# Optimization experiments

Hardware: AMD Instinct MI355X
Metric: run time of the kernel (lower is better)

The kernel has to match this reference:

```python
import jax, jax.numpy as jnp
import numpy as np

HEAD_NUM = 16
KEY_DIM = 64
EMBED = 1024
KV_OUT = HEAD_NUM * KEY_DIM  # 1024


def setup_inputs() -> dict:
    key = jax.random.key(0)
    ks = jax.random.split(key, 11)
    B, L, E = 2, 2048, EMBED
    scale = 0.02
    return {
        "query": jax.random.normal(ks[0], (B, L, E), jnp.float32),
        "key": jax.random.normal(ks[1], (B, L, E), jnp.float32),
        "value": jax.random.normal(ks[2], (B, L, E), jnp.float32),
        "W_Query": jax.random.normal(ks[3], (E, KV_OUT), jnp.float32) * scale,
        "W_Key": jax.random.normal(ks[4], (E, KV_OUT), jnp.float32) * scale,
        "W_Value": jax.random.normal(ks[5], (E, KV_OUT), jnp.float32) * scale,
        "W_Output": jax.random.normal(ks[6], (KV_OUT, E), jnp.float32) * scale,
        "B_Query": jnp.zeros((KV_OUT,), jnp.float32),
        "B_Key": jnp.zeros((KV_OUT,), jnp.float32),
        "B_Value": jnp.zeros((KV_OUT,), jnp.float32),
        "B_Output": jnp.zeros((E,), jnp.float32),
    }


def reference(query, key, value, W_Query, W_Key, W_Value, W_Output,
              B_Query, B_Key, B_Value, B_Output):
    B, Lq, E = query.shape
    Lk = key.shape[1]
    H, D = HEAD_NUM, KEY_DIM
    # QKV projections + bias
    q = query @ W_Query + B_Query            # [B, Lq, H*D]
    k = key @ W_Key + B_Key                  # [B, Lk, H*D]
    v = value @ W_Value + B_Value            # [B, Lk, H*D]
    # tf.split(axis=2) per head == reshape to [B, L, H, D]
    q = q.reshape(B, Lq, H, D)
    k = k.reshape(B, Lk, H, D)
    v = v.reshape(B, Lk, H, D)
    # scaled dot-product attention (no mask, dropout=0)
    scores = jnp.einsum("bqhd,bkhd->bhqk", q, k) / (D ** 0.5)
    probs = jax.nn.softmax(scores, axis=-1)
    out = jnp.einsum("bhqk,bkhd->bqhd", probs, v)  # [B, Lq, H, D]
    out = out.reshape(B, Lq, H * D)
    return out @ W_Output + B_Output
```

## Files before the change

kernel.cpp:

```cpp
#include <hip/hip_runtime.h>

using u16 = unsigned short;
using u32 = unsigned int;

typedef __attribute__((ext_vector_type(8))) short bf16x8;
typedef __attribute__((ext_vector_type(4))) float f32x4;
typedef __attribute__((ext_vector_type(4))) u32 u32x4;
typedef __attribute__((ext_vector_type(2))) u32 u32x2;
typedef __attribute__((ext_vector_type(4))) _Float16 f16x4;

#define MFMA_BF16_K32(a, b, c) __builtin_amdgcn_mfma_f32_16x16x32_bf16((a), (b), (c), 0, 0, 0)
#define MFMA_F16_K16(a, b, c) __builtin_amdgcn_mfma_f32_16x16x16f16((a), (b), (c), 0, 0, 0)

#define QSCALE 0.18033688011112042f

extern "C" __device__ float __ocml_native_exp2_f32(float);

__device__ __forceinline__ u16 f2bf(float f) {
  u32 u = __builtin_bit_cast(u32, f);
  return (u16)((u + 0x7fffu + ((u >> 16) & 1u)) >> 16);
}

__device__ __forceinline__ u32 pk_f16(float a, float b) {
  auto v = __builtin_amdgcn_cvt_pkrtz(a, b);
  return __builtin_bit_cast(u32, v);
}

__device__ __forceinline__ void load_lds16(const void* g, void* l) {
  __builtin_amdgcn_global_load_lds((__attribute__((address_space(1))) void*)g,
                                   (__attribute__((address_space(3))) void*)l,
                                   16, 0, 0);
}

__global__ __launch_bounds__(256) void cvt_all_kernel(
    const float* __restrict__ q, const float* __restrict__ k, const float* __restrict__ v,
    u16* __restrict__ oq, u16* __restrict__ ok, u16* __restrict__ ov,
    const float* __restrict__ w0, const float* __restrict__ w1,
    const float* __restrict__ w2, const float* __restrict__ w3,
    u16* __restrict__ d0, u16* __restrict__ d1,
    u16* __restrict__ d2, u16* __restrict__ d3) {
  const int id = blockIdx.x;
  const int tid = threadIdx.x;
  if (id < 6144) {
    const int z = id >> 11, bx = id & 2047;
    const float* s = z == 0 ? q : z == 1 ? k : v;
    u16* d = z == 0 ? oq : z == 1 ? ok : ov;
    int i = (bx * 256 + tid) * 8;
    f32x4 a = *(const f32x4*)(s + i);
    f32x4 b = *(const f32x4*)(s + i + 4);
    u32x4 o;
    o.x = (u32)f2bf(a.x) | ((u32)f2bf(a.y) << 16);
    o.y = (u32)f2bf(a.z) | ((u32)f2bf(a.w) << 16);
    o.z = (u32)f2bf(b.x) | ((u32)f2bf(b.y) << 16);
    o.w = (u32)f2bf(b.z) | ((u32)f2bf(b.w) << 16);
    *(u32x4*)(d + i) = o;
    return;
  }
  __shared__ float t[64][65];
  const int r0 = id - 6144;
  const int z = r0 >> 8, rr0 = r0 & 255;
  const int bx = rr0 & 15, by = rr0 >> 4;
  const float* src = z == 0 ? w0 : z == 1 ? w1 : z == 2 ? w2 : w3;
  u16* dst = z == 0 ? d0 : z == 1 ? d1 : z == 2 ? d2 : d3;
  const float scale = (z == 0) ? QSCALE : 1.0f;
  const int r = tid >> 4, c4 = (tid & 15) * 4;
#pragma unroll
  for (int i = 0; i < 4; ++i) {
    int row = r + i * 16;
    f32x4 vv = *(const f32x4*)(src + (by * 64 + row) * 1024 + bx * 64 + c4);
    t[row][c4 + 0] = vv.x;
    t[row][c4 + 1] = vv.y;
    t[row][c4 + 2] = vv.z;
    t[row][c4 + 3] = vv.w;
  }
  __syncthreads();
  const int rw = tid >> 2, cc = (tid & 3) * 16;
  alignas(16) u16 tmp[16];
#pragma unroll
  for (int j = 0; j < 16; ++j) tmp[j] = f2bf(t[cc + j][rw] * scale);
  u32x4* outp = (u32x4*)(dst + (bx * 64 + rw) * 1024 + by * 64 + cc);
  outp[0] = *(const u32x4*)&tmp[0];
  outp[1] = *(const u32x4*)&tmp[8];
}

__global__ __launch_bounds__(256) void gemm_qkv_kernel(
    const u16* __restrict__ x0, const u16* __restrict__ x1, const u16* __restrict__ x2,
    const u16* __restrict__ w0, const u16* __restrict__ w1, const u16* __restrict__ w2,
    const float* __restrict__ b0, const float* __restrict__ b1, const float* __restrict__ b2,
    u16* __restrict__ c0, u16* __restrict__ c1, u16* __restrict__ vt) {
  __shared__ u16 As[128 * 64];
  __shared__ u16 Bs[128 * 64];
  const int lid = blockIdx.x;
  const int xcd = lid & 7, rr = lid >> 3;
  const int nb = rr & 7, slot = rr >> 3;
  const int g = slot * 8 + xcd;
  const int z = g >> 5, m_idx = g & 31;
  const u16* A = z == 0 ? x0 : z == 1 ? x1 : x2;
  const u16* Bt = z == 0 ? w0 : z == 1 ? w1 : w2;
  const float* bias = z == 0 ? b0 : z == 1 ? b1 : b2;
  const float bscale = z == 0 ? QSCALE : 1.0f;
  const int tid = threadIdx.x;
  const int wave = tid >> 6, lane = tid & 63;
  const int l16 = lane & 15, quad = lane >> 4;
  const int l7 = l16 & 7;
  const int wm = wave >> 1, wn = wave & 1;
  const int m0 = m_idx * 128, n0 = nb * 128;

  f32x4 acc[4][4];
  const f32x4 zf = {0.f, 0.f, 0.f, 0.f};
#pragma unroll
  for (int i = 0; i < 4; ++i)
#pragma unroll
    for (int j = 0; j < 4; ++j) acc[i][j] = zf;

  for (int kb = 0; kb < 1024; kb += 64) {
#pragma unroll
    for (int t = 0; t < 4; ++t) {
      int c = wave * 256 + t * 64 + lane;
      int row = c >> 3, sc8 = (c & 7) ^ (row & 7);
      load_lds16(A + (m0 + row) * 1024 + kb + sc8 * 8, &As[(wave * 256 + t * 64) * 8]);
    }
#pragma unroll
    for (int t = 0; t < 4; ++t) {
      int c = wave * 256 + t * 64 + lane;
      int row = c >> 3, sc8 = (c & 7) ^ (row & 7);
      load_lds16(Bt + (n0 + row) * 1024 + kb + sc8 * 8, &Bs[(wave * 256 + t * 64) * 8]);
    }
    asm volatile("s_waitcnt vmcnt(0)" ::: "memory");
    __syncthreads();
#pragma unroll
    for (int ks = 0; ks < 2; ++ks) {
      const int sch = (ks * 4 + quad) ^ l7;
      bf16x8 af[4], bfv[4];
#pragma unroll
      for (int mt = 0; mt < 4; ++mt)
        af[mt] = *(const bf16x8*)&As[(wm * 64 + mt * 16 + l16) * 64 + sch * 8];
#pragma unroll
      for (int nt = 0; nt < 4; ++nt)
        bfv[nt] = *(const bf16x8*)&Bs[(wn * 64 + nt * 16 + l16) * 64 + sch * 8];
#pragma unroll
      for (int mt = 0; mt < 4; ++mt)
#pragma unroll
        for (int nt = 0; nt < 4; ++nt) acc[mt][nt] = MFMA_BF16_K32(af[mt], bfv[nt], acc[mt][nt]);
    }
    __syncthreads();
  }

  float bv[4];
#pragma unroll
  for (int nt = 0; nt < 4; ++nt) bv[nt] = bias[n0 + wn * 64 + nt * 16 + l16] * bscale;
  if (z != 2) {
    u16* C = z == 0 ? c0 : c1;
#pragma unroll
    for (int mt = 0; mt < 4; ++mt)
#pragma unroll
      for (int nt = 0; nt < 4; ++nt)
#pragma unroll
        for (int r = 0; r < 4; ++r) {
          int row = m0 + wm * 64 + mt * 16 + quad * 4 + r;
          int col = n0 + wn * 64 + nt * 16 + l16;
          C[row * 1024 + col] = f2bf(acc[mt][nt][r] + bv[nt]);
        }
  } else {
#pragma unroll
    for (int mt = 0; mt < 4; ++mt)
#pragma unroll
      for (int nt = 0; nt < 4; ++nt) {
        int kvb = m0 + wm * 64 + mt * 16 + quad * 4;
        int bb = kvb >> 11, kv = kvb & 2047;
        int col = n0 + wn * 64 + nt * 16 + l16;
        int h = col >> 6, dt = (col >> 4) & 3, ld = col & 15;
        int pair = bb * 16 + h;
        int kb2 = kv >> 7, chunk = (kv >> 4) & 7, qd = (kv >> 2) & 3;
        f16x4 hv;
#pragma unroll
        for (int r = 0; r < 4; ++r) hv[r] = (_Float16)(acc[mt][nt][r] + bv[nt]);
        u16* dst = vt + ((((pair * 16 + kb2) * 8 + chunk) * 4 + dt) * 256) + qd * 64 + ld * 4;
        *(f16x4*)dst = hv;
      }
  }
}

__global__ __launch_bounds__(256) void gemm_out_kernel(const u16* __restrict__ A,
                                                       const u16* __restrict__ Bt,
                                                       const float* __restrict__ bias,
                                                       float* __restrict__ C) {
  __shared__ u16 As[64 * 64];
  __shared__ u16 Bs[128 * 64];
  const int lid = blockIdx.x;
  const int xcd = lid & 7, rr = lid >> 3;
  const int nb = rr & 7, slot = rr >> 3;
  const int by = slot * 8 + xcd;
  const int tid = threadIdx.x;
  const int wave = tid >> 6, lane = tid & 63;
  const int l16 = lane & 15, quad = lane >> 4;
  const int l7 = l16 & 7;
  const int m0 = by * 64, n0 = nb * 128;

  f32x4 acc[4][2];
  const f32x4 zf = {0.f, 0.f, 0.f, 0.f};
#pragma unroll
  for (int i = 0; i < 4; ++i)
#pragma unroll
    for (int j = 0; j < 2; ++j) acc[i][j] = zf;

  for (int kb = 0; kb < 1024; kb += 64) {
#pragma unroll
    for (int t = 0; t < 2; ++t) {
      int c = wave * 128 + t * 64 + lane;
      int row = c >> 3, sc8 = (c & 7) ^ (row & 7);
      load_lds16(A + (m0 + row) * 1024 + kb + sc8 * 8, &As[(wave * 128 + t * 64) * 8]);
    }
#pragma unroll
    for (int t = 0; t < 4; ++t) {
      int c = wave * 256 + t * 64 + lane;
      int row = c >> 3, sc8 = (c & 7) ^ (row & 7);
      load_lds16(Bt + (n0 + row) * 1024 + kb + sc8 * 8, &Bs[(wave * 256 + t * 64) * 8]);
    }
    asm volatile("s_waitcnt vmcnt(0)" ::: "memory");
    __syncthreads();
#pragma unroll
    for (int ks = 0; ks < 2; ++ks) {
      const int sch = (ks * 4 + quad) ^ l7;
      bf16x8 af[4], bfv[2];
#pragma unroll
      for (int mt = 0; mt < 4; ++mt)
        af[mt] = *(const bf16x8*)&As[(mt * 16 + l16) * 64 + sch * 8];
#pragma unroll
      for (int nt = 0; nt < 2; ++nt)
        bfv[nt] = *(const bf16x8*)&Bs[(wave * 32 + nt * 16 + l16) * 64 + sch * 8];
#pragma unroll
      for (int mt = 0; mt < 4; ++mt)
#pragma unroll
        for (int nt = 0; nt < 2; ++nt) acc[mt][nt] = MFMA_BF16_K32(af[mt], bfv[nt], acc[mt][nt]);
    }
    __syncthreads();
  }

  float bv[2];
#pragma unroll
  for (int nt = 0; nt < 2; ++nt) bv[nt] = bias[n0 + wave * 32 + nt * 16 + l16];
#pragma unroll
  for (int mt = 0; mt < 4; ++mt)
#pragma unroll
    for (int nt = 0; nt < 2; ++nt)
#pragma unroll
      for (int r = 0; r < 4; ++r) {
        int row = m0 + mt * 16 + quad * 4 + r;
        int col = n0 + wave * 32 + nt * 16 + l16;
        C[row * 1024 + col] = acc[mt][nt][r] + bv[nt];
      }
}

union PU { u32 u[2]; f16x4 v; };

#define QK_EXP(CUR, PKV)                                                          \
  _Pragma("unroll") for (int c2 = 0; c2 < 2; ++c2) {                              \
    const int chunk = wave * 2 + c2;                                              \
    f32x4 s_acc[4];                                                               \
    _Pragma("unroll") for (int qn = 0; qn < 4; ++qn) s_acc[qn] = zf;              \
    _Pragma("unroll") for (int ks = 0; ks < 2; ++ks) {                            \
      bf16x8 kf = *(const bf16x8*)&k_lds[CUR][(chunk * 16 + l16) * 64 +           \
                                              ((ks * 4 + quad) ^ l7) * 8];        \
      _Pragma("unroll") for (int qn = 0; qn < 4; ++qn)                            \
        s_acc[qn] = MFMA_BF16_K32(kf, qf[qn][ks], s_acc[qn]);                     \
    }                                                                             \
    _Pragma("unroll") for (int qn = 0; qn < 4; ++qn) {                            \
      float e0 = __ocml_native_exp2_f32(s_acc[qn].x);                             \
      float e1 = __ocml_native_exp2_f32(s_acc[qn].y);                             \
      float e2 = __ocml_native_exp2_f32(s_acc[qn].z);                             \
      float e3 = __ocml_native_exp2_f32(s_acc[qn].w);                             \
      lp[qn] += (e0 + e1) + (e2 + e3);                                            \
      PKV[c2][qn].u[0] = pk_f16(e0, e1);                                          \
      PKV[c2][qn].u[1] = pk_f16(e2, e3);                                          \
    }                                                                             \
  }

#define FLASH_BODY(KB, CUR, VCUR, VNXT, PFV, PFK, WAIT)                           \
  {                                                                               \
    __builtin_amdgcn_s_barrier();                                                 \
    asm volatile("" ::: "memory");                                                \
    if (PFV) {                                                                    \
      const u16* vp = Vh + ((KB) + 1) * 8192;                                     \
      _Pragma("unroll") for (int c2 = 0; c2 < 2; ++c2)                            \
        _Pragma("unroll") for (int dt = 0; dt < 4; ++dt)                          \
          VNXT[c2][dt] =                                                          \
              *(const f16x4*)(vp + ((wave * 2 + c2) * 4 + dt) * 256 + lane * 4);  \
    }                                                                             \
    PU pkv[2][4];                                                                 \
    QK_EXP(CUR, pkv)                                                              \
    asm volatile("s_waitcnt lgkmcnt(0)" ::: "memory");                            \
    __builtin_amdgcn_s_barrier();                                                 \
    asm volatile("" ::: "memory");                                                \
    if (PFK) {                                                                    \
      const int kv0 = ((KB) + 2) * 128;                                           \
      _Pragma("unroll") for (int t = 0; t < 4; ++t) {                             \
        int c = (t * 4 + wave) * 64 + lane;                                       \
        int row = c >> 3, sc8 = (c & 7) ^ (row & 7);                              \
        load_lds16(Kh + (kv0 + row) * 1024 + sc8 * 8,                             \
                   &k_lds[CUR][((t * 4 + wave) * 64) * 8]);                       \
      }                                                                           \
    }                                                                             \
    WAIT;                                                                         \
    _Pragma("unroll") for (int c2 = 0; c2 < 2; ++c2)                              \
      _Pragma("unroll") for (int dt = 0; dt < 4; ++dt)                            \
        _Pragma("unroll") for (int qn = 0; qn < 4; ++qn)                          \
          o_acc[qn][dt] = MFMA_F16_K16(pkv[c2][qn].v, VCUR[c2][dt], o_acc[qn][dt]); \
  }

#define W12 asm volatile("s_waitcnt vmcnt(12)" ::: "memory")
#define W8 asm volatile("s_waitcnt vmcnt(8)" ::: "memory")
#define W0 asm volatile("s_waitcnt vmcnt(0)" ::: "memory")

__global__ __launch_bounds__(256, 2) void flash_kernel(const u16* __restrict__ Q,
                                                       const u16* __restrict__ K,
                                                       const u16* __restrict__ Vt,
                                                       u16* __restrict__ O) {
  __shared__ u16 k_lds[2][128 * 64];
  __shared__ float lred[4][64];
  __shared__ float lfin[64];
  const int tid = threadIdx.x;
  const int wave = tid >> 6, lane = tid & 63;
  const int l16 = lane & 15, quad = lane >> 4;
  const int l7 = l16 & 7;
  const int id = blockIdx.x;
  const int xcd = id & 7, slot = id >> 3;
  const int pair = xcd * 4 + (slot & 3);
  const int qb = slot >> 2;
  const int b = pair >> 4, h = pair & 15;
  const u16* Qh = Q + (b * 2048 + qb * 64) * 1024 + h * 64;
  const u16* Kh = K + b * 2048 * 1024 + h * 64;
  const u16* Vh = Vt + pair * 131072;

#pragma unroll
  for (int t = 0; t < 2; ++t) {
    int c = (t * 4 + wave) * 64 + lane;
    int row = c >> 3, sc8 = (c & 7) ^ (row & 7);
    load_lds16(Qh + row * 1024 + sc8 * 8, &k_lds[0][((t * 4 + wave) * 64) * 8]);
  }
  asm volatile("s_waitcnt vmcnt(0)" ::: "memory");
  __syncthreads();
  bf16x8 qf[4][2];
#pragma unroll
  for (int qn = 0; qn < 4; ++qn)
#pragma unroll
    for (int ks = 0; ks < 2; ++ks)
      qf[qn][ks] = *(const bf16x8*)&k_lds[0][(qn * 16 + l16) * 64 + (((ks * 4 + quad) ^ l7)) * 8];
  __syncthreads();

#pragma unroll
  for (int t = 0; t < 4; ++t) {
    int c = (t * 4 + wave) * 64 + lane;
    int row = c >> 3, sc8 = (c & 7) ^ (row & 7);
    load_lds16(Kh + row * 1024 + sc8 * 8, &k_lds[0][((t * 4 + wave) * 64) * 8]);
  }
  f16x4 vregA[2][4], vregB[2][4];
#pragma unroll
  for (int c2 = 0; c2 < 2; ++c2)
#pragma unroll
    for (int dt = 0; dt < 4; ++dt)
      vregA[c2][dt] = *(const f16x4*)(Vh + ((wave * 2 + c2) * 4 + dt) * 256 + lane * 4);
#pragma unroll
  for (int t = 0; t < 4; ++t) {
    int c = (t * 4 + wave) * 64 + lane;
    int row = c >> 3, sc8 = (c & 7) ^ (row & 7);
    load_lds16(Kh + (128 + row) * 1024 + sc8 * 8, &k_lds[1][((t * 4 + wave) * 64) * 8]);
  }
  W12;

  f32x4 o_acc[4][4];
  const f32x4 zf = {0.f, 0.f, 0.f, 0.f};
#pragma unroll
  for (int qn = 0; qn < 4; ++qn)
#pragma unroll
    for (int dt = 0; dt < 4; ++dt) o_acc[qn][dt] = zf;
  float lp[4] = {0.f, 0.f, 0.f, 0.f};

  for (int kb2 = 0; kb2 < 7; ++kb2) {
    const int kb = kb2 * 2;
    FLASH_BODY(kb, 0, vregA, vregB, true, true, W12);
    FLASH_BODY(kb + 1, 1, vregB, vregA, true, true, W12);
  }
  FLASH_BODY(14, 0, vregA, vregB, true, false, W8);
  FLASH_BODY(15, 1, vregB, vregA, false, false, W0);

#pragma unroll
  for (int qn = 0; qn < 4; ++qn) {
    lp[qn] += __shfl_xor(lp[qn], 16);
    lp[qn] += __shfl_xor(lp[qn], 32);
  }
  if (quad == 0) {
#pragma unroll
    for (int qn = 0; qn < 4; ++qn) lred[wave][qn * 16 + l16] = lp[qn];
  }
  float* bufA = (float*)&k_lds[0][0];
  float* bufB = (float*)&k_lds[1][0];
  if (wave == 1 || wave == 3) {
    float* buf = (wave == 1) ? bufA : bufB;
#pragma unroll
    for (int qm = 0; qm < 4; ++qm)
#pragma unroll
      for (int dt = 0; dt < 4; ++dt)
        *(f32x4*)&buf[(((qm * 4 + dt) * 4 + quad) * 16 + l16) * 4] = o_acc[qm][dt];
  }
  __syncthreads();
  if (tid < 64) lfin[tid] = lred[0][tid] + lred[1][tid] + lred[2][tid] + lred[3][tid];
  if (wave == 0 || wave == 2) {
    float* buf = (wave == 0) ? bufA : bufB;
#pragma unroll
    for (int qm = 0; qm < 4; ++qm)
#pragma unroll
      for (int dt = 0; dt < 4; ++dt)
        o_acc[qm][dt] += *(const f32x4*)&buf[(((qm * 4 + dt) * 4 + quad) * 16 + l16) * 4];
  }
  __syncthreads();
  if (wave == 2) {
#pragma unroll
    for (int qm = 0; qm < 4; ++qm)
#pragma unroll
      for (int dt = 0; dt < 4; ++dt)
        *(f32x4*)&bufA[(((qm * 4 + dt) * 4 + quad) * 16 + l16) * 4] = o_acc[qm][dt];
  }
  __syncthreads();
  if (wave == 0) {
#pragma unroll
    for (int qm = 0; qm < 4; ++qm)
#pragma unroll
      for (int dt = 0; dt < 4; ++dt)
        o_acc[qm][dt] += *(const f32x4*)&bufA[(((qm * 4 + dt) * 4 + quad) * 16 + l16) * 4];
#pragma unroll
    for (int qm = 0; qm < 4; ++qm)
#pragma unroll
      for (int r = 0; r < 4; ++r) {
        int qrow = qm * 16 + quad * 4 + r;
        float inv = 1.0f / lfin[qrow];
        int row = b * 2048 + qb * 64 + qrow;
#pragma unroll
        for (int dt = 0; dt < 4; ++dt)
          O[row * 1024 + h * 64 + dt * 16 + l16] = f2bf(o_acc[qm][dt][r] * inv);
      }
  }
}

extern "C" void kernel_launch(void* const* d_in, const int* in_sizes, int n_in,
                              void* d_out, int out_size, void* d_ws, size_t ws_size,
                              hipStream_t stream) {
  const float* q = (const float*)d_in[0];
  const float* k = (const float*)d_in[1];
  const float* v = (const float*)d_in[2];
  const float* Wq = (const float*)d_in[3];
  const float* Wk = (const float*)d_in[4];
  const float* Wv = (const float*)d_in[5];
  const float* Wo = (const float*)d_in[6];
  const float* Bq = (const float*)d_in[7];
  const float* Bk = (const float*)d_in[8];
  const float* Bv = (const float*)d_in[9];
  const float* Bo = (const float*)d_in[10];
  float* out = (float*)d_out;

  char* w = (char*)d_ws;
  const size_t MB = 1u << 20;
  u16* xq = (u16*)(w + 0 * MB);
  u16* xk = (u16*)(w + 8 * MB);
  u16* xv = (u16*)(w + 16 * MB);
  u16* wqt = (u16*)(w + 24 * MB);
  u16* wkt = (u16*)(w + 26 * MB);
  u16* wvt = (u16*)(w + 28 * MB);
  u16* wot = (u16*)(w + 30 * MB);
  u16* Qp = (u16*)(w + 32 * MB);
  u16* Kp = (u16*)(w + 40 * MB);
  u16* Vtr = (u16*)(w + 48 * MB);
  u16* At = (u16*)(w + 56 * MB);

  cvt_all_kernel<<<dim3(7168), 256, 0, stream>>>(q, k, v, xq, xk, xv,
                                                 Wq, Wk, Wv, Wo, wqt, wkt, wvt, wot);
  gemm_qkv_kernel<<<dim3(768), 256, 0, stream>>>(xq, xk, xv, wqt, wkt, wvt,
                                                 Bq, Bk, Bv, Qp, Kp, Vtr);
  flash_kernel<<<dim3(1024), 256, 0, stream>>>(Qp, Kp, Vtr, At);
  gemm_out_kernel<<<dim3(512), 256, 0, stream>>>(At, wot, Bo, out);
}
```

Before: 225.9 us.

## Double-buffer LDS in QKV and output GEMMs with async prefetch

Both projection GEMMs move from a single-buffered 64-wide K tile, which waited on all global loads before computing, to a two-stage 32-wide K tile ring. The loads for step kb+2 are issued right after the compute on step kb, with partial vmcnt waits. This is meant to hide global-to-LDS latency behind MFMA work. The swizzle is changed to suit 32-wide rows, and each iteration now has two barriers and half as many MFMAs, which adds more synchronization per unit of work.

```diff
diff --git a/kernel.cpp b/kernel.cpp
--- a/kernel.cpp
+++ b/kernel.cpp
@@ -31,6 +31,18 @@
                                    (__attribute__((address_space(3))) void*)l,
                                    16, 0, 0);
 }
+
+#define W0 asm volatile("s_waitcnt vmcnt(0)" ::: "memory")
+#define W3 asm volatile("s_waitcnt vmcnt(3)" ::: "memory")
+#define W4 asm volatile("s_waitcnt vmcnt(4)" ::: "memory")
+#define W8 asm volatile("s_waitcnt vmcnt(8)" ::: "memory")
+#define W12 asm volatile("s_waitcnt vmcnt(12)" ::: "memory")
+#define LGKM0 asm volatile("s_waitcnt lgkmcnt(0)" ::: "memory")
+#define BARRIER                      \
+  do {                               \
+    __builtin_amdgcn_s_barrier();    \
+    asm volatile("" ::: "memory");   \
+  } while (0)
 
 __global__ __launch_bounds__(256) void cvt_all_kernel(
     const float* __restrict__ q, const float* __restrict__ k, const float* __restrict__ v,
@@ -83,13 +95,29 @@
   outp[1] = *(const u32x4*)&tmp[8];
 }
 
+#define QKV_STAGE(BUF, KB)                                                    \
+  {                                                                           \
+    _Pragma("unroll") for (int t = 0; t < 2; ++t) {                           \
+      int c = (wave * 2 + t) * 64 + lane;                                     \
+      int row = c >> 2, pc = c & 3, sc = pc ^ ((row >> 1) & 3);               \
+      load_lds16(A + (m0 + row) * 1024 + (KB) * 32 + sc * 8,                  \
+                 &As[BUF][((wave * 2 + t) * 64) * 8]);                        \
+    }                                                                         \
+    _Pragma("unroll") for (int t = 0; t < 2; ++t) {                           \
+      int c = (wave * 2 + t) * 64 + lane;                                     \
+      int row = c >> 2, pc = c & 3, sc = pc ^ ((row >> 1) & 3);               \
+      load_lds16(Bt + (n0 + row) * 1024 + (KB) * 32 + sc * 8,                 \
+                 &Bs[BUF][((wave * 2 + t) * 64) * 8]);                        \
+    }                                                                         \
+  }
+
 __global__ __launch_bounds__(256) void gemm_qkv_kernel(
     const u16* __restrict__ x0, const u16* __restrict__ x1, const u16* __restrict__ x2,
     const u16* __restrict__ w0, const u16* __restrict__ w1, const u16* __restrict__ w2,
     const float* __restrict__ b0, const float* __restrict__ b1, const float* __restrict__ b2,
     u16* __restrict__ c0, u16* __restrict__ c1, u16* __restrict__ vt) {
-  __shared__ u16 As[128 * 64];
-  __shared__ u16 Bs[128 * 64];
+  __shared__ u16 As[2][128 * 32];
+  __shared__ u16 Bs[2][128 * 32];
   const int lid = blockIdx.x;
   const int xcd = lid & 7, rr = lid >> 3;
   const int nb = rr & 7, slot = rr >> 3;
@@ -102,7 +130,6 @@
   const int tid = threadIdx.x;
   const int wave = tid >> 6, lane = tid & 63;
   const int l16 = lane & 15, quad = lane >> 4;
-  const int l7 = l16 & 7;
   const int wm = wave >> 1, wn = wave & 1;
   const int m0 = m_idx * 128, n0 = nb * 128;
 
@@ -113,37 +140,28 @@
 #pragma unroll
     for (int j = 0; j < 4; ++j) acc[i][j] = zf;
 
-  for (int kb = 0; kb < 1024; kb += 64) {
-#pragma unroll
-    for (int t = 0; t < 4; ++t) {
-      int c = wave * 256 + t * 64 + lane;
-      int row = c >> 3, sc8 = (c & 7) ^ (row & 7);
-      load_lds16(A + (m0 + row) * 1024 + kb + sc8 * 8, &As[(wave * 256 + t * 64) * 8]);
-    }
-#pragma unroll
-    for (int t = 0; t < 4; ++t) {
-      int c = wave * 256 + t * 64 + lane;
-      int row = c >> 3, sc8 = (c & 7) ^ (row & 7);
-      load_lds16(Bt + (n0 + row) * 1024 + kb + sc8 * 8, &Bs[(wave * 256 + t * 64) * 8]);
-    }
-    asm volatile("s_waitcnt vmcnt(0)" ::: "memory");
-    __syncthreads();
-#pragma unroll
-    for (int ks = 0; ks < 2; ++ks) {
-      const int sch = (ks * 4 + quad) ^ l7;
-      bf16x8 af[4], bfv[4];
-#pragma unroll
-      for (int mt = 0; mt < 4; ++mt)
-        af[mt] = *(const bf16x8*)&As[(wm * 64 + mt * 16 + l16) * 64 + sch * 8];
-#pragma unroll
-      for (int nt = 0; nt < 4; ++nt)
-        bfv[nt] = *(const bf16x8*)&Bs[(wn * 64 + nt * 16 + l16) * 64 + sch * 8];
-#pragma unroll
-      for (int mt = 0; mt < 4; ++mt)
-#pragma unroll
-        for (int nt = 0; nt < 4; ++nt) acc[mt][nt] = MFMA_BF16_K32(af[mt], bfv[nt], acc[mt][nt]);
-    }
-    __syncthreads();
+  QKV_STAGE(0, 0);
+  QKV_STAGE(1, 1);
+
+  const int chq = (l16 >> 1) & 3;
+  for (int kb = 0; kb < 32; ++kb) {
+    const int cur = kb & 1;
+    if (kb < 31) W4; else W0;
+    BARRIER;
+    bf16x8 af[4], bfv[4];
+#pragma unroll
+    for (int mt = 0; mt < 4; ++mt)
+      af[mt] = *(const bf16x8*)&As[cur][(wm * 64 + mt * 16 + l16) * 32 + (quad ^ chq) * 8];
+#pragma unroll
+    for (int nt = 0; nt < 4; ++nt)
+      bfv[nt] = *(const bf16x8*)&Bs[cur][(wn * 64 + nt * 16 + l16) * 32 + (quad ^ chq) * 8];
+#pragma unroll
+    for (int mt = 0; mt < 4; ++mt)
+#pragma unroll
+      for (int nt = 0; nt < 4; ++nt) acc[mt][nt] = MFMA_BF16_K32(af[mt], bfv[nt], acc[mt][nt]);
+    LGKM0;
+    BARRIER;
+    if (kb + 2 < 32) QKV_STAGE(cur, kb + 2);
   }
 
   float bv[4];
@@ -181,12 +199,28 @@
   }
 }
 
+#define OUT_STAGE(BUF, KB)                                                    \
+  {                                                                           \
+    {                                                                         \
+      int c = wave * 64 + lane;                                               \
+      int row = c >> 2, pc = c & 3, sc = pc ^ ((row >> 1) & 3);               \
+      load_lds16(A + (m0 + row) * 1024 + (KB) * 32 + sc * 8,                  \
+                 &As[BUF][(wave * 64) * 8]);                                  \
+    }                                                                         \
+    _Pragma("unroll") for (int t = 0; t < 2; ++t) {                           \
+      int c = (wave * 2 + t) * 64 + lane;                                     \
+      int row = c >> 2, pc = c & 3, sc = pc ^ ((row >> 1) & 3);               \
+      load_lds16(Bt + (n0 + row) * 1024 + (KB) * 32 + sc * 8,                 \
+                 &Bs[BUF][((wave * 2 + t) * 64) * 8]);                        \
+    }                                                                         \
+  }
+
 __global__ __launch_bounds__(256) void gemm_out_kernel(const u16* __restrict__ A,
                                                        const u16* __restrict__ Bt,
                                                        const float* __restrict__ bias,
                                                        float* __restrict__ C) {
-  __shared__ u16 As[64 * 64];
-  __shared__ u16 Bs[128 * 64];
+  __shared__ u16 As[2][64 * 32];
+  __shared__ u16 Bs[2][128 * 32];
   const int lid = blockIdx.x;
   const int xcd = lid & 7, rr = lid >> 3;
   const int nb = rr & 7, slot = rr >> 3;
@@ -194,7 +228,6 @@
   const int tid = threadIdx.x;
   const int wave = tid >> 6, lane = tid & 63;
   const int l16 = lane & 15, quad = lane >> 4;
-  const int l7 = l16 & 7;
   const int m0 = by * 64, n0 = nb * 128;
 
   f32x4 acc[4][2];
@@ -204,37 +237,28 @@
 #pragma unroll
     for (int j = 0; j < 2; ++j) acc[i][j] = zf;
 
-  for (int kb = 0; kb < 1024; kb += 64) {
-#pragma unroll
-    for (int t = 0; t < 2; ++t) {
-      int c = wave * 128 + t * 64 + lane;
-      int row = c >> 3, sc8 = (c & 7) ^ (row & 7);
-      load_lds16(A + (m0 + row) * 1024 + kb + sc8 * 8, &As[(wave * 128 + t * 64) * 8]);
-    }
-#pragma unroll
-    for (int t = 0; t < 4; ++t) {
-      int c = wave * 256 + t * 64 + lane;
-      int row = c >> 3, sc8 = (c & 7) ^ (row & 7);
-      load_lds16(Bt + (n0 + row) * 1024 + kb + sc8 * 8, &Bs[(wave * 256 + t * 64) * 8]);
-    }
-    asm volatile("s_waitcnt vmcnt(0)" ::: "memory");
-    __syncthreads();
-#pragma unroll
-    for (int ks = 0; ks < 2; ++ks) {
-      const int sch = (ks * 4 + quad) ^ l7;
-      bf16x8 af[4], bfv[2];
-#pragma unroll
-      for (int mt = 0; mt < 4; ++mt)
-        af[mt] = *(const bf16x8*)&As[(mt * 16 + l16) * 64 + sch * 8];
-#pragma unroll
-      for (int nt = 0; nt < 2; ++nt)
-        bfv[nt] = *(const bf16x8*)&Bs[(wave * 32 + nt * 16 + l16) * 64 + sch * 8];
-#pragma unroll
-      for (int mt = 0; mt < 4; ++mt)
-#pragma unroll
-        for (int nt = 0; nt < 2; ++nt) acc[mt][nt] = MFMA_BF16_K32(af[mt], bfv[nt], acc[mt][nt]);
-    }
-    __syncthreads();
+  OUT_STAGE(0, 0);
+  OUT_STAGE(1, 1);
+
+  const int chq = (l16 >> 1) & 3;
+  for (int kb = 0; kb < 32; ++kb) {
+    const int cur = kb & 1;
+    if (kb < 31) W3; else W0;
+    BARRIER;
+    bf16x8 af[4], bfv[2];
+#pragma unroll
+    for (int mt = 0; mt < 4; ++mt)
+      af[mt] = *(const bf16x8*)&As[cur][(mt * 16 + l16) * 32 + (quad ^ chq) * 8];
+#pragma unroll
+    for (int nt = 0; nt < 2; ++nt)
+      bfv[nt] = *(const bf16x8*)&Bs[cur][(wave * 32 + nt * 16 + l16) * 32 + (quad ^ chq) * 8];
+#pragma unroll
+    for (int mt = 0; mt < 4; ++mt)
+#pragma unroll
+      for (int nt = 0; nt < 2; ++nt) acc[mt][nt] = MFMA_BF16_K32(af[mt], bfv[nt], acc[mt][nt]);
+    LGKM0;
+    BARRIER;
+    if (kb + 2 < 32) OUT_STAGE(cur, kb + 2);
   }
 
   float bv[2];
@@ -278,8 +302,7 @@
 
 #define FLASH_BODY(KB, CUR, VCUR, VNXT, PFV, PFK, WAIT)                           \
   {                                                                               \
-    __builtin_amdgcn_s_barrier();                                                 \
-    asm volatile("" ::: "memory");                                                \
+    BARRIER;                                                                      \
     if (PFV) {                                                                    \
       const u16* vp = Vh + ((KB) + 1) * 8192;                                     \
       _Pragma("unroll") for (int c2 = 0; c2 < 2; ++c2)                            \
@@ -289,9 +312,8 @@
     }                                                                             \
     PU pkv[2][4];                                                                 \
     QK_EXP(CUR, pkv)                                                              \
-    asm volatile("s_waitcnt lgkmcnt(0)" ::: "memory");                            \
-    __builtin_amdgcn_s_barrier();                                                 \
-    asm volatile("" ::: "memory");                                                \
+    LGKM0;                                                                        \
+    BARRIER;                                                                      \
     if (PFK) {                                                                    \
       const int kv0 = ((KB) + 2) * 128;                                           \
       _Pragma("unroll") for (int t = 0; t < 4; ++t) {                             \
@@ -307,10 +329,6 @@
         _Pragma("unroll") for (int qn = 0; qn < 4; ++qn)                          \
           o_acc[qn][dt] = MFMA_F16_K16(pkv[c2][qn].v, VCUR[c2][dt], o_acc[qn][dt]); \
   }
-
-#define W12 asm volatile("s_waitcnt vmcnt(12)" ::: "memory")
-#define W8 asm volatile("s_waitcnt vmcnt(8)" ::: "memory")
-#define W0 asm volatile("s_waitcnt vmcnt(0)" ::: "memory")
 
 __global__ __launch_bounds__(256, 2) void flash_kernel(const u16* __restrict__ Q,
                                                        const u16* __restrict__ K,
@@ -338,7 +356,7 @@
     int row = c >> 3, sc8 = (c & 7) ^ (row & 7);
     load_lds16(Qh + row * 1024 + sc8 * 8, &k_lds[0][((t * 4 + wave) * 64) * 8]);
   }
-  asm volatile("s_waitcnt vmcnt(0)" ::: "memory");
+  W0;
   __syncthreads();
   bf16x8 qf[4][2];
 #pragma unroll
```

Result: faster. 218.0 us (-3.5%).
